# Optimization experiments

Hardware: AMD Instinct MI355X
Metric: run time of the kernel (lower is better)

## Reference

```python
import jax, jax.numpy as jnp
import numpy as np

P = 16           # patch size
D = 768          # embed / feature dim (= 3*P*P)
T = 8            # number of task vectors
H_META = 192     # MetaNet hidden (= D // 4)


def patchify(x):
    # x: [B, 3, H, W] -> [B, N, 3*P*P]
    B, C, H, W = x.shape
    x = x.reshape(B, C, H // P, P, W // P, P)
    x = x.transpose(0, 2, 4, 1, 3, 5)
    return x.reshape(B, (H // P) * (W // P), C * P * P)


def encode(W1, b1, W2, b2, x):
    # base functional encoder f(params, x): shared weights over the batch
    patches = patchify(x)                       # [B, N, D]
    h = jax.nn.relu(patches @ W1 + b1)          # [B, N, D]
    pooled = h.mean(axis=1)                     # [B, D]
    return pooled @ W2 + b2                     # [B, D]


def setup_inputs() -> dict:
    key = jax.random.key(0)
    ks = jax.random.split(key, 14)
    B = 64
    s = 0.02
    return {
        "x":   jax.random.normal(ks[0], (B, 3, 224, 224), jnp.float32),
        # base model params
        "W1":  jax.random.normal(ks[1], (D, D), jnp.float32) * s,
        "b1":  jax.random.normal(ks[2], (D,), jnp.float32) * s,
        "W2":  jax.random.normal(ks[3], (D, D), jnp.float32) * s,
        "b2":  jax.random.normal(ks[4], (D,), jnp.float32) * s,
        # task-vector deltas (stacked over T tasks)
        "dW1": jax.random.normal(ks[5], (T, D, D), jnp.float32) * s,
        "db1": jax.random.normal(ks[6], (T, D), jnp.float32) * s,
        "dW2": jax.random.normal(ks[7], (T, D, D), jnp.float32) * s,
        "db2": jax.random.normal(ks[8], (T, D), jnp.float32) * s,
        # MetaNet (Linear-ReLU-Linear); zero-init in the original, random here
        "mw1": jax.random.normal(ks[9], (D, H_META), jnp.float32) * s,
        "mb1": jax.random.normal(ks[10], (H_META,), jnp.float32) * s,
        "mw2": jax.random.normal(ks[11], (H_META, T), jnp.float32) * s,
        "mb2": jax.random.normal(ks[12], (T,), jnp.float32) * s,
    }


def reference(x, W1, b1, W2, b2, dW1, db1, dW2, db2, mw1, mb1, mw2, mb2):
    # 1) base features with frozen base model (torch.no_grad)
    base = jax.lax.stop_gradient(encode(W1, b1, W2, b2, x))       # [B, D]
    # 2) per-sample mixing coefficients via MetaNet
    coefs = jax.nn.relu(base @ mw1 + mb1) @ mw2 + mb2             # [B, T]
    # 3) per-sample mixed parameters: p + sum_t c[b,t] * dp[t]
    nW1 = W1 + jnp.einsum("bt,tij->bij", coefs, dW1)              # [B, D, D]
    nb1 = b1 + coefs @ db1                                        # [B, D]
    nW2 = W2 + jnp.einsum("bt,tij->bij", coefs, dW2)              # [B, D, D]
    nb2 = b2 + coefs @ db2                                        # [B, D]
    # 4) batched per-sample forward with the mixed weights
    patches = patchify(x)                                         # [B, N, D]
    h = jax.nn.relu(jnp.einsum("bnd,bde->bne", patches, nW1) + nb1[:, None, :])
    pooled = h.mean(axis=1)                                       # [B, D]
    out = jnp.einsum("bd,bde->be", pooled, nW2) + nb2             # [B, D]
    return out
```

## Files before the change

kernel.cpp:

```cpp
#include <hip/hip_runtime.h>
#include <hip/hip_bf16.h>


typedef __bf16 bf16x8 __attribute__((ext_vector_type(8)));
typedef float f32x4 __attribute__((ext_vector_type(4)));
typedef __hip_bfloat16 bf16;

struct alignas(16) BF8 { bf16 h[8]; };

constexpr int BATCH = 64;
constexpr int NP    = 196;
constexpr int NPAD  = 256;
constexpr int DIM   = 768;
constexpr int NT    = 8;
constexpr size_t MSZ = (size_t)DIM * DIM;

__device__ __forceinline__ void async_cp16(const void* g, void* l) {
  __builtin_amdgcn_global_load_lds(
      (const __attribute__((address_space(1))) uint32_t*)g,
      (__attribute__((address_space(3))) uint32_t*)l, 16, 0, 0);
}

__global__ void k_patchify(const float* __restrict__ x, bf16* __restrict__ A) {
  int idx  = blockIdx.x * blockDim.x + threadIdx.x;
  int col4 = idx % (DIM / 4);
  int row  = idx / (DIM / 4);
  int d = col4 * 4;
  int b = row >> 8;
  int n = row & 255;
  bf16 tmp[4];
  if (n < NP) {
    int hp = n / 14, wp = n % 14;
    int c  = d >> 8;
    int rr = d & 255;
    int i = rr >> 4, j = rr & 15;
    const float* src = x + ((((size_t)b * 3 + c) * 224 + hp * 16 + i) * 224 + wp * 16 + j);
    float4 f = *(const float4*)src;
    tmp[0] = __float2bfloat16(f.x);
    tmp[1] = __float2bfloat16(f.y);
    tmp[2] = __float2bfloat16(f.z);
    tmp[3] = __float2bfloat16(f.w);
  } else {
    tmp[0] = tmp[1] = tmp[2] = tmp[3] = __float2bfloat16(0.0f);
  }
  *(ushort4*)(A + (size_t)row * DIM + d) = *(ushort4*)tmp;
}

__global__ void k_transpose_cast(const float* __restrict__ W1, const float* __restrict__ dW1,
                                 const float* __restrict__ W2, const float* __restrict__ dW2,
                                 bf16* __restrict__ WT) {
  __shared__ float tile[32][33];
  int mat = blockIdx.z;
  const float* src;
  if      (mat == 0) src = W1;
  else if (mat <= 8) src = dW1 + (size_t)(mat - 1) * MSZ;
  else if (mat == 9) src = W2;
  else               src = dW2 + (size_t)(mat - 10) * MSZ;
  int n0 = blockIdx.x * 32;
  int k0 = blockIdx.y * 32;
  int tx = threadIdx.x & 31, ty = threadIdx.x >> 5;
#pragma unroll
  for (int r = ty; r < 32; r += 8)
    tile[r][tx] = src[(size_t)(k0 + r) * DIM + n0 + tx];
  __syncthreads();
  bf16* dst = WT + (size_t)mat * MSZ;
#pragma unroll
  for (int r = ty; r < 32; r += 8)
    dst[(size_t)(n0 + r) * DIM + k0 + tx] = __float2bfloat16(tile[tx][r]);
}


#define WAITVM(N) asm volatile("s_waitcnt vmcnt(" #N ")" ::: "memory")

template<int MIX>
__global__ __launch_bounds__(256, 3)
void k_gemm_pool(const bf16* __restrict__ A,
                 const bf16* __restrict__ WT,
                 const float* __restrict__ b1,
                 const float* __restrict__ db1,
                 const float* __restrict__ coefs,
                 float* __restrict__ pooled) {
  __shared__ uint4 AslU[3][896];
  __shared__ uint4 BslU[2][256];

  int b  = blockIdx.x;
  int n0 = blockIdx.y * 64;
  int tid = threadIdx.x;
  int wave = tid >> 6, lane = tid & 63;
  int quad = lane >> 4, l16 = lane & 15;

  float cr[NT];
  if (MIX) {
#pragma unroll
    for (int t = 0; t < NT; t++) cr[t] = coefs[b * NT + t];
  }

  const bf16* Ag = A + (size_t)b * NPAD * DIM;
  f32x4 acc[4][4] = {};

  int gbase = (wave < 2) ? wave * 256 : 512 + (wave - 2) * 192;
  int gcnt  = (wave < 2) ? 4 : 3;
  auto stage_a = [&](int buf, int kt) {
    const bf16* Ak = Ag + kt * 32;
#pragma unroll
    for (int i = 0; i < 4; i++) {
      if (i < gcnt) {
        int s = gbase + i * 64 + lane;
        int p = s >> 3, u = (s & 7) ^ (p & 7);
        int r = 2 * p + (u >> 2), c = u & 3;
        async_cp16(Ak + (size_t)r * DIM + c * 8, (void*)&AslU[buf][gbase + i * 64]);
      }
    }
  };

  int bp = tid >> 3, bu = (tid & 7) ^ (bp & 7);
  int brow_st = 2 * bp + (bu >> 2), bcol_st = bu & 3;
  const bf16* Wrow = WT + (size_t)(n0 + brow_st) * DIM + bcol_st * 8;

  BF8 wreg[MIX ? 9 : 1];
  auto breg_load = [&](int kt) {
    const bf16* p0 = Wrow + kt * 32;
    wreg[0] = *(const BF8*)p0;
    if (MIX) {
#pragma unroll
      for (int t = 0; t < NT; t++)
        wreg[1 + t] = *(const BF8*)(p0 + (size_t)(1 + t) * MSZ);
    }
  };
  auto breg_write = [&](int buf) {
    if (MIX) {
      float m[8];
#pragma unroll
      for (int j = 0; j < 8; j++) m[j] = __bfloat162float(wreg[0].h[j]);
#pragma unroll
      for (int t = 0; t < NT; t++) {
        float cc = cr[t];
#pragma unroll
        for (int j = 0; j < 8; j++) m[j] += cc * __bfloat162float(wreg[1 + t].h[j]);
      }
      BF8 o;
#pragma unroll
      for (int j = 0; j < 8; j++) o.h[j] = __float2bfloat16(m[j]);
      BslU[buf][tid] = *(uint4*)&o;
    } else {
      BslU[buf][tid] = *(uint4*)&wreg[0];
    }
  };

  auto gslot = [&](int row, int kq) {
    return (size_t)((row >> 1) * 8 + ((4 * (row & 1) + kq) ^ ((row >> 1) & 7)));
  };

  stage_a(0, 0);
  stage_a(1, 1);
  breg_load(0);
  WAITVM(0);
  __builtin_amdgcn_sched_barrier(0);
  breg_write(0);
  asm volatile("s_waitcnt lgkmcnt(0)" ::: "memory");

  int bufA = 0, stgA = 2, bufB = 0;
  for (int kt = 0; kt < 24; kt++) {
    __builtin_amdgcn_s_barrier();
    if (kt < 23) breg_load(kt + 1);
    __builtin_amdgcn_sched_barrier(0);
    if (kt < 22) stage_a(stgA, kt + 2);
    __builtin_amdgcn_sched_barrier(0);
    const bf16* As = (const bf16*)AslU[bufA];
    const bf16* Bs = (const bf16*)BslU[bufB];
    bf16x8 bfr[4];
#pragma unroll
    for (int nf = 0; nf < 4; nf++) {
      int brow = nf * 16 + l16;
      bfr[nf] = *(const bf16x8*)(Bs + gslot(brow, quad) * 8);
    }
#pragma unroll
    for (int mf = 0; mf < 4; mf++) {
      if (wave * 64 + mf * 16 < 224) {
        int arow = wave * 64 + mf * 16 + l16;
        bf16x8 af = *(const bf16x8*)(As + gslot(arow, quad) * 8);
#pragma unroll
        for (int nf = 0; nf < 4; nf++)
          acc[mf][nf] = __builtin_amdgcn_mfma_f32_16x16x32_bf16(af, bfr[nf], acc[mf][nf], 0, 0, 0);
      }
    }
    if (kt < 22) {
      if (wave < 2) WAITVM(4); else WAITVM(3);
    } else if (kt < 23) {
      WAITVM(0);
    }
    __builtin_amdgcn_sched_barrier(0);
    if (kt < 23) {
      breg_write(bufB ^ 1);
      asm volatile("s_waitcnt lgkmcnt(0)" ::: "memory");
    }
    bufA = (bufA == 2) ? 0 : bufA + 1;
    stgA = (stgA == 2) ? 0 : stgA + 1;
    bufB ^= 1;
  }

  float* red = (float*)&BslU[0][0];
  int m0 = wave * 64;
  float colsum[4];
#pragma unroll
  for (int nf = 0; nf < 4; nf++) {
    int col = n0 + nf * 16 + l16;
    float bias = b1[col];
    if (MIX) {
#pragma unroll
      for (int t = 0; t < NT; t++) bias += cr[t] * db1[t * DIM + col];
    }
    float s = 0.0f;
#pragma unroll
    for (int mf = 0; mf < 4; mf++) {
      int rbase = m0 + mf * 16 + quad * 4;
#pragma unroll
      for (int r = 0; r < 4; r++) {
        if (rbase + r < NP) s += fmaxf(acc[mf][nf][r] + bias, 0.0f);
      }
    }
    s += __shfl_xor(s, 16, 64);
    s += __shfl_xor(s, 32, 64);
    colsum[nf] = s;
  }
  if (lane < 16) {
#pragma unroll
    for (int nf = 0; nf < 4; nf++) red[wave * 64 + nf * 16 + lane] = colsum[nf];
  }
  __syncthreads();
  if (tid < 64) {
    float s = red[tid] + red[64 + tid] + red[128 + tid] + red[192 + tid];
    pooled[(size_t)b * DIM + n0 + tid] = s * (1.0f / 196.0f);
  }
}

__global__ __launch_bounds__(256, 2)
void k_gemm2(const float* __restrict__ Af,
             const bf16* __restrict__ WT,
             int matbase,
             const float* __restrict__ bias,
             float* __restrict__ Y) {
  __shared__ uint4 AslU[64 * 8];
  __shared__ uint4 BslU[64 * 8];
  int n0  = blockIdx.x * 64;
  int mat = blockIdx.y;
  int tid = threadIdx.x, wave = tid >> 6, lane = tid & 63;
  int quad = lane >> 4, l16 = lane & 15;
  f32x4 acc[4] = {};
  const bf16* Wm = WT + (size_t)(matbase + mat) * MSZ;
  for (int k0 = 0; k0 < DIM; k0 += 64) {
#pragma unroll
    for (int i = 0; i < 2; i++) {
      int g = tid + i * 256;
      int r = g >> 3, c = g & 7;
      const float* src = Af + (size_t)r * DIM + k0 + c * 8;
      float4 xa = ((const float4*)src)[0];
      float4 xb = ((const float4*)src)[1];
      BF8 o;
      o.h[0] = __float2bfloat16(xa.x); o.h[1] = __float2bfloat16(xa.y);
      o.h[2] = __float2bfloat16(xa.z); o.h[3] = __float2bfloat16(xa.w);
      o.h[4] = __float2bfloat16(xb.x); o.h[5] = __float2bfloat16(xb.y);
      o.h[6] = __float2bfloat16(xb.z); o.h[7] = __float2bfloat16(xb.w);
      AslU[r * 8 + (c ^ (r & 7))] = *(uint4*)&o;
      BslU[r * 8 + (c ^ (r & 7))] = *(const uint4*)(Wm + (size_t)(n0 + r) * DIM + k0 + c * 8);
    }
    __syncthreads();
    const bf16* As = (const bf16*)AslU;
    const bf16* Bs = (const bf16*)BslU;
#pragma unroll
    for (int ks = 0; ks < 2; ks++) {
      int brow = wave * 16 + l16;
      bf16x8 bfr = *(const bf16x8*)(Bs + (size_t)(brow * 8 + ((ks * 4 + quad) ^ (brow & 7))) * 8);
#pragma unroll
      for (int mf = 0; mf < 4; mf++) {
        int arow = mf * 16 + l16;
        bf16x8 af = *(const bf16x8*)(As + (size_t)(arow * 8 + ((ks * 4 + quad) ^ (arow & 7))) * 8);
        acc[mf] = __builtin_amdgcn_mfma_f32_16x16x32_bf16(af, bfr, acc[mf], 0, 0, 0);
      }
    }
    __syncthreads();
  }
#pragma unroll
  for (int mf = 0; mf < 4; mf++) {
#pragma unroll
    for (int r = 0; r < 4; r++) {
      int row = mf * 16 + quad * 4 + r;
      int col = n0 + wave * 16 + l16;
      float v = acc[mf][r];
      if (bias) v += bias[col];
      Y[((size_t)mat * 64 + row) * DIM + col] = v;
    }
  }
}

__global__ void k_metanet(const float* __restrict__ base,
                          const float* __restrict__ mw1, const float* __restrict__ mb1,
                          const float* __restrict__ mw2, const float* __restrict__ mb2,
                          float* __restrict__ coefs) {
  __shared__ float bl[DIM];
  __shared__ float hl[192];
  int b = blockIdx.x, tid = threadIdx.x;
  for (int i = tid; i < DIM; i += 192) bl[i] = base[(size_t)b * DIM + i];
  __syncthreads();
  float s = mb1[tid];
  for (int k = 0; k < DIM; k++) s += bl[k] * mw1[(size_t)k * 192 + tid];
  hl[tid] = fmaxf(s, 0.0f);
  __syncthreads();
  if (tid < NT) {
    float c = mb2[tid];
    for (int j = 0; j < 192; j++) c += hl[j] * mw2[(size_t)j * NT + tid];
    coefs[b * NT + tid] = c;
  }
}

__global__ void k_combine(const float* __restrict__ Y,
                          const float* __restrict__ coefs,
                          const float* __restrict__ b2,
                          const float* __restrict__ db2,
                          float* __restrict__ out) {
  int idx = blockIdx.x * 256 + threadIdx.x;
  int b = idx / DIM, e = idx % DIM;
  float v = Y[(size_t)b * DIM + e] + b2[e];
#pragma unroll
  for (int t = 0; t < NT; t++) {
    float c = coefs[b * NT + t];
    v += c * (Y[((size_t)(1 + t) * 64 + b) * DIM + e] + db2[(size_t)t * DIM + e]);
  }
  out[idx] = v;
}

extern "C" void kernel_launch(void* const* d_in, const int* in_sizes, int n_in,
                              void* d_out, int out_size, void* d_ws, size_t ws_size,
                              hipStream_t stream) {
  const float* x   = (const float*)d_in[0];
  const float* W1  = (const float*)d_in[1];
  const float* b1  = (const float*)d_in[2];
  const float* W2  = (const float*)d_in[3];
  const float* b2  = (const float*)d_in[4];
  const float* dW1 = (const float*)d_in[5];
  const float* db1 = (const float*)d_in[6];
  const float* dW2 = (const float*)d_in[7];
  const float* db2 = (const float*)d_in[8];
  const float* mw1 = (const float*)d_in[9];
  const float* mb1 = (const float*)d_in[10];
  const float* mw2 = (const float*)d_in[11];
  const float* mb2 = (const float*)d_in[12];
  float* out = (float*)d_out;
  (void)in_sizes; (void)n_in; (void)out_size; (void)ws_size;

  char* ws = (char*)d_ws;
  bf16*  A_bf    = (bf16*) (ws);
  bf16*  WT      = (bf16*) (ws + 25165824);
  float* pooledA = (float*)(ws + 46399488);
  float* pooledB = (float*)(ws + 46596096);
  float* coefs   = (float*)(ws + 46792704);
  float* base    = (float*)(ws + 46794752);
  float* Y       = (float*)(ws + 46991360);

  k_patchify<<<dim3((BATCH * NPAD * (DIM / 4)) / 256), 256, 0, stream>>>(x, A_bf);
  k_transpose_cast<<<dim3(24, 24, 18), 256, 0, stream>>>(W1, dW1, W2, dW2, WT);
  k_gemm_pool<0><<<dim3(BATCH, DIM / 64), 256, 0, stream>>>(A_bf, WT, b1, db1, nullptr, pooledA);
  k_gemm2<<<dim3(DIM / 64, 1), 256, 0, stream>>>(pooledA, WT, 9, b2, base);
  k_metanet<<<dim3(BATCH), 192, 0, stream>>>(base, mw1, mb1, mw2, mb2, coefs);
  k_gemm_pool<1><<<dim3(BATCH, DIM / 64), 256, 0, stream>>>(A_bf, WT, b1, db1, coefs, pooledB);
  k_gemm2<<<dim3(DIM / 64, 9), 256, 0, stream>>>(pooledB, WT, 9, nullptr, Y);
  k_combine<<<dim3((BATCH * DIM) / 256), 256, 0, stream>>>(Y, coefs, b2, db2, out);
}
```

Measured before the change: 297.4 us.

## Fuse base GEMM with MetaNet, split-K final GEMM, prioritize MFMA waves

Replaces the small base-feature GEMM plus the separate MetaNet launch with one per-sample kernel that computes base features from bf16 W2 and then the coefficients, removing a launch and an intermediate buffer. The final per-task GEMM is split along K into two halves to double the number of blocks, and the combine kernel sums the two partial results. The main GEMM precomputes A-staging offsets once per thread and raises wave priority around the MFMA loop. The fused base kernel computes the dot products with scalar FP32 code rather than matrix cores, and the split-K adds extra Y traffic in exchange for more parallelism.

```diff
diff --git a/kernel.cpp b/kernel.cpp
--- a/kernel.cpp
+++ b/kernel.cpp
@@ -3,6 +3,7 @@
 
 
 typedef __bf16 bf16x8 __attribute__((ext_vector_type(8)));
+typedef unsigned short u16x8 __attribute__((ext_vector_type(8)));
 typedef float f32x4 __attribute__((ext_vector_type(4)));
 typedef __hip_bfloat16 bf16;
 
@@ -100,16 +101,20 @@
 
   int gbase = (wave < 2) ? wave * 256 : 512 + (wave - 2) * 192;
   int gcnt  = (wave < 2) ? 4 : 3;
+  int aoff[4];
+#pragma unroll
+  for (int i = 0; i < 4; i++) {
+    int s = gbase + i * 64 + lane;
+    int p = s >> 3, u = (s & 7) ^ (p & 7);
+    int r = 2 * p + (u >> 2), c = u & 3;
+    aoff[i] = r * DIM + c * 8;
+  }
   auto stage_a = [&](int buf, int kt) {
     const bf16* Ak = Ag + kt * 32;
 #pragma unroll
     for (int i = 0; i < 4; i++) {
-      if (i < gcnt) {
-        int s = gbase + i * 64 + lane;
-        int p = s >> 3, u = (s & 7) ^ (p & 7);
-        int r = 2 * p + (u >> 2), c = u & 3;
-        async_cp16(Ak + (size_t)r * DIM + c * 8, (void*)&AslU[buf][gbase + i * 64]);
-      }
+      if (i < gcnt)
+        async_cp16(Ak + aoff[i], (void*)&AslU[buf][gbase + i * 64]);
     }
   };
 
@@ -174,6 +179,7 @@
       int brow = nf * 16 + l16;
       bfr[nf] = *(const bf16x8*)(Bs + gslot(brow, quad) * 8);
     }
+    __builtin_amdgcn_s_setprio(1);
 #pragma unroll
     for (int mf = 0; mf < 4; mf++) {
       if (wave * 64 + mf * 16 < 224) {
@@ -184,6 +190,7 @@
           acc[mf][nf] = __builtin_amdgcn_mfma_f32_16x16x32_bf16(af, bfr[nf], acc[mf][nf], 0, 0, 0);
       }
     }
+    __builtin_amdgcn_s_setprio(0);
     if (kt < 22) {
       if (wave < 2) WAITVM(4); else WAITVM(3);
     } else if (kt < 23) {
@@ -234,21 +241,61 @@
   }
 }
 
+__global__ __launch_bounds__(256)
+void k_base_coefs(const float* __restrict__ pooledA,
+                  const bf16* __restrict__ WT,
+                  const float* __restrict__ b2,
+                  const float* __restrict__ mw1, const float* __restrict__ mb1,
+                  const float* __restrict__ mw2, const float* __restrict__ mb2,
+                  float* __restrict__ coefs) {
+  __shared__ float pl[DIM];
+  __shared__ float bs[DIM];
+  __shared__ float hl[192];
+  int b = blockIdx.x, tid = threadIdx.x;
+  for (int i = tid; i < DIM; i += 256) pl[i] = pooledA[(size_t)b * DIM + i];
+  __syncthreads();
+  const bf16* W2T = WT + (size_t)9 * MSZ;
+#pragma unroll
+  for (int o = 0; o < 3; o++) {
+    int n = o * 256 + tid;
+    const bf16* wr = W2T + (size_t)n * DIM;
+    float s = b2[n];
+    for (int k = 0; k < DIM; k += 8) {
+      u16x8 w = *(const u16x8*)(wr + k);
+#pragma unroll
+      for (int j = 0; j < 8; j++)
+        s += pl[k + j] * __uint_as_float((unsigned)w[j] << 16);
+    }
+    bs[n] = s;
+  }
+  __syncthreads();
+  if (tid < 192) {
+    float s = mb1[tid];
+    for (int k = 0; k < DIM; k++) s += bs[k] * mw1[(size_t)k * 192 + tid];
+    hl[tid] = fmaxf(s, 0.0f);
+  }
+  __syncthreads();
+  if (tid < NT) {
+    float c = mb2[tid];
+    for (int j = 0; j < 192; j++) c += hl[j] * mw2[(size_t)j * NT + tid];
+    coefs[b * NT + tid] = c;
+  }
+}
+
 __global__ __launch_bounds__(256, 2)
 void k_gemm2(const float* __restrict__ Af,
              const bf16* __restrict__ WT,
-             int matbase,
-             const float* __restrict__ bias,
              float* __restrict__ Y) {
   __shared__ uint4 AslU[64 * 8];
   __shared__ uint4 BslU[64 * 8];
   int n0  = blockIdx.x * 64;
   int mat = blockIdx.y;
+  int kz  = blockIdx.z;
   int tid = threadIdx.x, wave = tid >> 6, lane = tid & 63;
   int quad = lane >> 4, l16 = lane & 15;
   f32x4 acc[4] = {};
-  const bf16* Wm = WT + (size_t)(matbase + mat) * MSZ;
-  for (int k0 = 0; k0 < DIM; k0 += 64) {
+  const bf16* Wm = WT + (size_t)(9 + mat) * MSZ;
+  for (int k0 = kz * 384; k0 < kz * 384 + 384; k0 += 64) {
 #pragma unroll
     for (int i = 0; i < 2; i++) {
       int g = tid + i * 256;
@@ -286,30 +333,8 @@
     for (int r = 0; r < 4; r++) {
       int row = mf * 16 + quad * 4 + r;
       int col = n0 + wave * 16 + l16;
-      float v = acc[mf][r];
-      if (bias) v += bias[col];
-      Y[((size_t)mat * 64 + row) * DIM + col] = v;
-    }
-  }
-}
-
-__global__ void k_metanet(const float* __restrict__ base,
-                          const float* __restrict__ mw1, const float* __restrict__ mb1,
-                          const float* __restrict__ mw2, const float* __restrict__ mb2,
-                          float* __restrict__ coefs) {
-  __shared__ float bl[DIM];
-  __shared__ float hl[192];
-  int b = blockIdx.x, tid = threadIdx.x;
-  for (int i = tid; i < DIM; i += 192) bl[i] = base[(size_t)b * DIM + i];
-  __syncthreads();
-  float s = mb1[tid];
-  for (int k = 0; k < DIM; k++) s += bl[k] * mw1[(size_t)k * 192 + tid];
-  hl[tid] = fmaxf(s, 0.0f);
-  __syncthreads();
-  if (tid < NT) {
-    float c = mb2[tid];
-    for (int j = 0; j < 192; j++) c += hl[j] * mw2[(size_t)j * NT + tid];
-    coefs[b * NT + tid] = c;
+      Y[(((size_t)kz * 9 + mat) * 64 + row) * DIM + col] = acc[mf][r];
+    }
   }
 }
 
@@ -320,11 +345,14 @@
                           float* __restrict__ out) {
   int idx = blockIdx.x * 256 + threadIdx.x;
   int b = idx / DIM, e = idx % DIM;
-  float v = Y[(size_t)b * DIM + e] + b2[e];
+  const size_t ZS = (size_t)9 * 64 * DIM;
+  size_t i0 = (size_t)b * DIM + e;
+  float v = Y[i0] + Y[ZS + i0] + b2[e];
 #pragma unroll
   for (int t = 0; t < NT; t++) {
     float c = coefs[b * NT + t];
-    v += c * (Y[((size_t)(1 + t) * 64 + b) * DIM + e] + db2[(size_t)t * DIM + e]);
+    size_t it = ((size_t)(1 + t) * 64 + b) * DIM + e;
+    v += c * (Y[it] + Y[ZS + it] + db2[(size_t)t * DIM + e]);
   }
   out[idx] = v;
 }
@@ -354,15 +382,13 @@
   float* pooledA = (float*)(ws + 46399488);
   float* pooledB = (float*)(ws + 46596096);
   float* coefs   = (float*)(ws + 46792704);
-  float* base    = (float*)(ws + 46794752);
-  float* Y       = (float*)(ws + 46991360);
+  float* Y       = (float*)(ws + 46794752);
 
   k_patchify<<<dim3((BATCH * NPAD * (DIM / 4)) / 256), 256, 0, stream>>>(x, A_bf);
   k_transpose_cast<<<dim3(24, 24, 18), 256, 0, stream>>>(W1, dW1, W2, dW2, WT);
   k_gemm_pool<0><<<dim3(BATCH, DIM / 64), 256, 0, stream>>>(A_bf, WT, b1, db1, nullptr, pooledA);
-  k_gemm2<<<dim3(DIM / 64, 1), 256, 0, stream>>>(pooledA, WT, 9, b2, base);
-  k_metanet<<<dim3(BATCH), 192, 0, stream>>>(base, mw1, mb1, mw2, mb2, coefs);
+  k_base_coefs<<<dim3(BATCH), 256, 0, stream>>>(pooledA, WT, b2, mw1, mb1, mw2, mb2, coefs);
   k_gemm_pool<1><<<dim3(BATCH, DIM / 64), 256, 0, stream>>>(A_bf, WT, b1, db1, coefs, pooledB);
-  k_gemm2<<<dim3(DIM / 64, 9), 256, 0, stream>>>(pooledB, WT, 9, nullptr, Y);
+  k_gemm2<<<dim3(DIM / 64, 9, 2), 256, 0, stream>>>(pooledB, WT, Y);
   k_combine<<<dim3((BATCH * DIM) / 256), 256, 0, stream>>>(Y, coefs, b2, db2, out);
 }
```

Measured after the change: 318.4 us. +7.1%, slower.

## Merge prep kernels, split-K base GEMM, hoist A offsets, raise MFMA priority

Applied to the files above, without the earlier changes.

Patchify and weight transpose-cast are merged into one launch so both run in a single grid and one launch gap disappears. The single-matrix base GEMM gets a new split-K kernel over four K chunks to raise block count from 12 to 48, and the partial sums plus bias are added inside the MetaNet kernel. The gemm_pool kernel precomputes A staging offsets outside the K loop and raises wave priority around the MFMA block. These are several independent small ideas, and the split-K path adds extra partial-sum traffic and a wider workspace layout.

```diff
diff --git a/kernel.cpp b/kernel.cpp
--- a/kernel.cpp
+++ b/kernel.cpp
@@ -21,52 +21,60 @@
       (__attribute__((address_space(3))) uint32_t*)l, 16, 0, 0);
 }
 
-__global__ void k_patchify(const float* __restrict__ x, bf16* __restrict__ A) {
-  int idx  = blockIdx.x * blockDim.x + threadIdx.x;
-  int col4 = idx % (DIM / 4);
-  int row  = idx / (DIM / 4);
-  int d = col4 * 4;
-  int b = row >> 8;
-  int n = row & 255;
-  bf16 tmp[4];
-  if (n < NP) {
-    int hp = n / 14, wp = n % 14;
-    int c  = d >> 8;
-    int rr = d & 255;
-    int i = rr >> 4, j = rr & 15;
-    const float* src = x + ((((size_t)b * 3 + c) * 224 + hp * 16 + i) * 224 + wp * 16 + j);
-    float4 f = *(const float4*)src;
-    tmp[0] = __float2bfloat16(f.x);
-    tmp[1] = __float2bfloat16(f.y);
-    tmp[2] = __float2bfloat16(f.z);
-    tmp[3] = __float2bfloat16(f.w);
+constexpr int PREP_PATCH_BLOCKS = (BATCH * NPAD * (DIM / 4)) / 256;
+constexpr int PREP_TRANS_BLOCKS = 24 * 24 * 18;
+
+__global__ void k_prep(const float* __restrict__ x, bf16* __restrict__ A,
+                       const float* __restrict__ W1, const float* __restrict__ dW1,
+                       const float* __restrict__ W2, const float* __restrict__ dW2,
+                       bf16* __restrict__ WT) {
+  __shared__ float tile[32][33];
+  int blk = blockIdx.x;
+  int tid = threadIdx.x;
+  if (blk < PREP_PATCH_BLOCKS) {
+    int idx  = blk * 256 + tid;
+    int col4 = idx % (DIM / 4);
+    int row  = idx / (DIM / 4);
+    int d = col4 * 4;
+    int b = row >> 8;
+    int n = row & 255;
+    bf16 tmp[4];
+    if (n < NP) {
+      int hp = n / 14, wp = n % 14;
+      int c  = d >> 8;
+      int rr = d & 255;
+      int i = rr >> 4, j = rr & 15;
+      const float* src = x + ((((size_t)b * 3 + c) * 224 + hp * 16 + i) * 224 + wp * 16 + j);
+      float4 f = *(const float4*)src;
+      tmp[0] = __float2bfloat16(f.x);
+      tmp[1] = __float2bfloat16(f.y);
+      tmp[2] = __float2bfloat16(f.z);
+      tmp[3] = __float2bfloat16(f.w);
+    } else {
+      tmp[0] = tmp[1] = tmp[2] = tmp[3] = __float2bfloat16(0.0f);
+    }
+    *(ushort4*)(A + (size_t)row * DIM + d) = *(ushort4*)tmp;
   } else {
-    tmp[0] = tmp[1] = tmp[2] = tmp[3] = __float2bfloat16(0.0f);
-  }
-  *(ushort4*)(A + (size_t)row * DIM + d) = *(ushort4*)tmp;
-}
-
-__global__ void k_transpose_cast(const float* __restrict__ W1, const float* __restrict__ dW1,
-                                 const float* __restrict__ W2, const float* __restrict__ dW2,
-                                 bf16* __restrict__ WT) {
-  __shared__ float tile[32][33];
-  int mat = blockIdx.z;
-  const float* src;
-  if      (mat == 0) src = W1;
-  else if (mat <= 8) src = dW1 + (size_t)(mat - 1) * MSZ;
-  else if (mat == 9) src = W2;
-  else               src = dW2 + (size_t)(mat - 10) * MSZ;
-  int n0 = blockIdx.x * 32;
-  int k0 = blockIdx.y * 32;
-  int tx = threadIdx.x & 31, ty = threadIdx.x >> 5;
-#pragma unroll
-  for (int r = ty; r < 32; r += 8)
-    tile[r][tx] = src[(size_t)(k0 + r) * DIM + n0 + tx];
-  __syncthreads();
-  bf16* dst = WT + (size_t)mat * MSZ;
-#pragma unroll
-  for (int r = ty; r < 32; r += 8)
-    dst[(size_t)(n0 + r) * DIM + k0 + tx] = __float2bfloat16(tile[tx][r]);
+    int tb  = blk - PREP_PATCH_BLOCKS;
+    int mat = tb / 576;
+    int rem = tb % 576;
+    int n0 = (rem % 24) * 32;
+    int k0 = (rem / 24) * 32;
+    const float* src;
+    if      (mat == 0) src = W1;
+    else if (mat <= 8) src = dW1 + (size_t)(mat - 1) * MSZ;
+    else if (mat == 9) src = W2;
+    else               src = dW2 + (size_t)(mat - 10) * MSZ;
+    int tx = tid & 31, ty = tid >> 5;
+#pragma unroll
+    for (int r = ty; r < 32; r += 8)
+      tile[r][tx] = src[(size_t)(k0 + r) * DIM + n0 + tx];
+    __syncthreads();
+    bf16* dst = WT + (size_t)mat * MSZ;
+#pragma unroll
+    for (int r = ty; r < 32; r += 8)
+      dst[(size_t)(n0 + r) * DIM + k0 + tx] = __float2bfloat16(tile[tx][r]);
+  }
 }
 
 
@@ -100,16 +108,20 @@
 
   int gbase = (wave < 2) ? wave * 256 : 512 + (wave - 2) * 192;
   int gcnt  = (wave < 2) ? 4 : 3;
+  int aoff[4];
+#pragma unroll
+  for (int i = 0; i < 4; i++) {
+    int s = gbase + i * 64 + lane;
+    int p = s >> 3, u = (s & 7) ^ (p & 7);
+    int r = 2 * p + (u >> 2), c = u & 3;
+    aoff[i] = r * DIM + c * 8;
+  }
   auto stage_a = [&](int buf, int kt) {
     const bf16* Ak = Ag + kt * 32;
 #pragma unroll
     for (int i = 0; i < 4; i++) {
-      if (i < gcnt) {
-        int s = gbase + i * 64 + lane;
-        int p = s >> 3, u = (s & 7) ^ (p & 7);
-        int r = 2 * p + (u >> 2), c = u & 3;
-        async_cp16(Ak + (size_t)r * DIM + c * 8, (void*)&AslU[buf][gbase + i * 64]);
-      }
+      if (i < gcnt)
+        async_cp16(Ak + aoff[i], (void*)&AslU[buf][gbase + i * 64]);
     }
   };
 
@@ -174,6 +186,7 @@
       int brow = nf * 16 + l16;
       bfr[nf] = *(const bf16x8*)(Bs + gslot(brow, quad) * 8);
     }
+    __builtin_amdgcn_s_setprio(1);
 #pragma unroll
     for (int mf = 0; mf < 4; mf++) {
       if (wave * 64 + mf * 16 < 224) {
@@ -184,6 +197,7 @@
           acc[mf][nf] = __builtin_amdgcn_mfma_f32_16x16x32_bf16(af, bfr[nf], acc[mf][nf], 0, 0, 0);
       }
     }
+    __builtin_amdgcn_s_setprio(0);
     if (kt < 22) {
       if (wave < 2) WAITVM(4); else WAITVM(3);
     } else if (kt < 23) {
@@ -231,6 +245,61 @@
   if (tid < 64) {
     float s = red[tid] + red[64 + tid] + red[128 + tid] + red[192 + tid];
     pooled[(size_t)b * DIM + n0 + tid] = s * (1.0f / 196.0f);
+  }
+}
+
+__global__ __launch_bounds__(256, 2)
+void k_gemm2_ksplit(const float* __restrict__ Af,
+                    const bf16* __restrict__ WT,
+                    float* __restrict__ basep) {
+  __shared__ uint4 AslU[64 * 8];
+  __shared__ uint4 BslU[64 * 8];
+  int n0  = blockIdx.x * 64;
+  int kz  = blockIdx.y;
+  int tid = threadIdx.x, wave = tid >> 6, lane = tid & 63;
+  int quad = lane >> 4, l16 = lane & 15;
+  f32x4 acc[4] = {};
+  const bf16* Wm = WT + (size_t)9 * MSZ;
+  for (int k0 = kz * 192; k0 < kz * 192 + 192; k0 += 64) {
+#pragma unroll
+    for (int i = 0; i < 2; i++) {
+      int g = tid + i * 256;
+      int r = g >> 3, c = g & 7;
+      const float* src = Af + (size_t)r * DIM + k0 + c * 8;
+      float4 xa = ((const float4*)src)[0];
+      float4 xb = ((const float4*)src)[1];
+      BF8 o;
+      o.h[0] = __float2bfloat16(xa.x); o.h[1] = __float2bfloat16(xa.y);
+      o.h[2] = __float2bfloat16(xa.z); o.h[3] = __float2bfloat16(xa.w);
+      o.h[4] = __float2bfloat16(xb.x); o.h[5] = __float2bfloat16(xb.y);
+      o.h[6] = __float2bfloat16(xb.z); o.h[7] = __float2bfloat16(xb.w);
+      AslU[r * 8 + (c ^ (r & 7))] = *(uint4*)&o;
+      BslU[r * 8 + (c ^ (r & 7))] = *(const uint4*)(Wm + (size_t)(n0 + r) * DIM + k0 + c * 8);
+    }
+    __syncthreads();
+    const bf16* As = (const bf16*)AslU;
+    const bf16* Bs = (const bf16*)BslU;
+#pragma unroll
+    for (int ks = 0; ks < 2; ks++) {
+      int brow = wave * 16 + l16;
+      bf16x8 bfr = *(const bf16x8*)(Bs + (size_t)(brow * 8 + ((ks * 4 + quad) ^ (brow & 7))) * 8);
+#pragma unroll
+      for (int mf = 0; mf < 4; mf++) {
+        int arow = mf * 16 + l16;
+        bf16x8 af = *(const bf16x8*)(As + (size_t)(arow * 8 + ((ks * 4 + quad) ^ (arow & 7))) * 8);
+        acc[mf] = __builtin_amdgcn_mfma_f32_16x16x32_bf16(af, bfr, acc[mf], 0, 0, 0);
+      }
+    }
+    __syncthreads();
+  }
+#pragma unroll
+  for (int mf = 0; mf < 4; mf++) {
+#pragma unroll
+    for (int r = 0; r < 4; r++) {
+      int row = mf * 16 + quad * 4 + r;
+      int col = n0 + wave * 16 + l16;
+      basep[((size_t)kz * 64 + row) * DIM + col] = acc[mf][r];
+    }
   }
 }
 
@@ -293,14 +362,19 @@
   }
 }
 
-__global__ void k_metanet(const float* __restrict__ base,
+__global__ void k_metanet(const float* __restrict__ basep,
+                          const float* __restrict__ b2,
                           const float* __restrict__ mw1, const float* __restrict__ mb1,
                           const float* __restrict__ mw2, const float* __restrict__ mb2,
                           float* __restrict__ coefs) {
   __shared__ float bl[DIM];
   __shared__ float hl[192];
   int b = blockIdx.x, tid = threadIdx.x;
-  for (int i = tid; i < DIM; i += 192) bl[i] = base[(size_t)b * DIM + i];
+  const size_t ZS = (size_t)64 * DIM;
+  for (int i = tid; i < DIM; i += 192) {
+    size_t o = (size_t)b * DIM + i;
+    bl[i] = basep[o] + basep[ZS + o] + basep[2 * ZS + o] + basep[3 * ZS + o] + b2[i];
+  }
   __syncthreads();
   float s = mb1[tid];
   for (int k = 0; k < DIM; k++) s += bl[k] * mw1[(size_t)k * 192 + tid];
@@ -354,14 +428,14 @@
   float* pooledA = (float*)(ws + 46399488);
   float* pooledB = (float*)(ws + 46596096);
   float* coefs   = (float*)(ws + 46792704);
-  float* base    = (float*)(ws + 46794752);
-  float* Y       = (float*)(ws + 46991360);
-
-  k_patchify<<<dim3((BATCH * NPAD * (DIM / 4)) / 256), 256, 0, stream>>>(x, A_bf);
-  k_transpose_cast<<<dim3(24, 24, 18), 256, 0, stream>>>(W1, dW1, W2, dW2, WT);
+  float* basep   = (float*)(ws + 46794752);
+  float* Y       = (float*)(ws + 47581184);
+
+  k_prep<<<dim3(PREP_PATCH_BLOCKS + PREP_TRANS_BLOCKS), 256, 0, stream>>>(
+      x, A_bf, W1, dW1, W2, dW2, WT);
   k_gemm_pool<0><<<dim3(BATCH, DIM / 64), 256, 0, stream>>>(A_bf, WT, b1, db1, nullptr, pooledA);
-  k_gemm2<<<dim3(DIM / 64, 1), 256, 0, stream>>>(pooledA, WT, 9, b2, base);
-  k_metanet<<<dim3(BATCH), 192, 0, stream>>>(base, mw1, mb1, mw2, mb2, coefs);
+  k_gemm2_ksplit<<<dim3(DIM / 64, 4), 256, 0, stream>>>(pooledA, WT, basep);
+  k_metanet<<<dim3(BATCH), 192, 0, stream>>>(basep, b2, mw1, mb1, mw2, mb2, coefs);
   k_gemm_pool<1><<<dim3(BATCH, DIM / 64), 256, 0, stream>>>(A_bf, WT, b1, db1, coefs, pooledB);
   k_gemm2<<<dim3(DIM / 64, 9), 256, 0, stream>>>(pooledB, WT, 9, nullptr, Y);
   k_combine<<<dim3((BATCH * DIM) / 256), 256, 0, stream>>>(Y, coefs, b2, db2, out);
```

New measurement: 285.2 us. 4.1% less time.
